# Kernel tuning notes

Hardware: AMD Instinct MI355X
Metric: run time of the kernel (lower is better)

Reference implementation:

```python
import jax, jax.numpy as jnp
import numpy as np
import math

D_MODEL = 1024
N_HEADS = 16
D_FF = 4096
D_K = D_MODEL // N_HEADS
B, S = 2, 2048
EPS = 1e-5


def _linear_params(key, fan_in, fan_out):
    kw, kb = jax.random.split(key)
    bound = 1.0 / math.sqrt(fan_in)
    W = jax.random.uniform(kw, (fan_out, fan_in), jnp.float32, -bound, bound)
    b = jax.random.uniform(kb, (fan_out,), jnp.float32, -bound, bound)
    return W, b


def setup_inputs() -> dict:
    key = jax.random.key(0)
    ks = jax.random.split(key, 8)
    x = jax.random.normal(ks[0], (B, S, D_MODEL), jnp.float32)
    # causal mask, broadcast over batch and heads; 0 -> masked
    mask = jnp.tril(jnp.ones((S, S), jnp.int32))[None, None, :, :]
    wq, bq = _linear_params(ks[1], D_MODEL, D_MODEL)
    wk, bk = _linear_params(ks[2], D_MODEL, D_MODEL)
    wv, bv = _linear_params(ks[3], D_MODEL, D_MODEL)
    wo, bo = _linear_params(ks[4], D_MODEL, D_MODEL)
    w1, b1 = _linear_params(ks[5], D_MODEL, D_FF)
    w2, b2 = _linear_params(ks[6], D_FF, D_MODEL)
    g1 = jnp.ones((D_MODEL,), jnp.float32)
    be1 = jnp.zeros((D_MODEL,), jnp.float32)
    g2 = jnp.ones((D_MODEL,), jnp.float32)
    be2 = jnp.zeros((D_MODEL,), jnp.float32)
    return dict(x=x, mask=mask, wq=wq, bq=bq, wk=wk, bk=bk, wv=wv, bv=bv,
                wo=wo, bo=bo, w1=w1, b1=b1, w2=w2, b2=b2,
                g1=g1, be1=be1, g2=g2, be2=be2)


def _layernorm(x, g, b):
    mu = jnp.mean(x, axis=-1, keepdims=True)
    var = jnp.mean(jnp.square(x - mu), axis=-1, keepdims=True)
    return (x - mu) * jax.lax.rsqrt(var + EPS) * g + b


def reference(x, mask, wq, bq, wk, bk, wv, bv, wo, bo, w1, b1, w2, b2, g1, be1, g2, be2):
    Bsz, Sl, _ = x.shape
    def heads(t):  # [B,S,D] -> [B,H,S,d_k]
        return t.reshape(Bsz, Sl, N_HEADS, D_K).transpose(0, 2, 1, 3)
    Q = heads(x @ wq.T + bq)
    K = heads(x @ wk.T + bk)
    V = heads(x @ wv.T + bv)
    scores = jnp.einsum('bhqd,bhkd->bhqk', Q, K) / math.sqrt(D_K)
    scores = jnp.where(mask == 0, jnp.float32(-1e9), scores)
    attn = jax.nn.softmax(scores, axis=-1)
    out = jnp.einsum('bhqk,bhkd->bhqd', attn, V)
    out = out.transpose(0, 2, 1, 3).reshape(Bsz, Sl, D_MODEL)
    attn_out = out @ wo.T + bo
    h = _layernorm(x + attn_out, g1, be1)  # dropout is identity in eval
    ff = jax.nn.relu(h @ w1.T + b1) @ w2.T + b2
    return _layernorm(h + ff, g2, be2)
```

## Files before the change

### kernel.cpp

```cpp
#include <hip/hip_runtime.h>
#include <hip/hip_bf16.h>


using f32x4 = __attribute__((ext_vector_type(4))) float;
using s16x8 = __attribute__((ext_vector_type(8))) short;

constexpr int D_MODEL = 1024;
constexpr int D_FF    = 4096;
constexpr int DK      = 64;
constexpr int BB      = 2;
constexpr int SS      = 2048;
constexpr int NTOK    = BB * SS;

#define QSCALE 0.18033688011112042f

__device__ __forceinline__ ushort f2bf(float f) {
    unsigned u = __float_as_uint(f);
    u += 0x7fffu + ((u >> 16) & 1u);
    return (ushort)(u >> 16);
}

__device__ __forceinline__ float ex2(float x) {
    float r;
    asm("v_exp_f32 %0, %1" : "=v"(r) : "v"(x));
    return r;
}

__device__ __forceinline__ void gload_lds16(const void* g, void* l) {
    __builtin_amdgcn_global_load_lds(
        (const __attribute__((address_space(1))) void*)g,
        (__attribute__((address_space(3))) void*)l, 16, 0, 0);
}

struct CvtArgs { const float* src[7]; ushort* dst[7]; };

__global__ __launch_bounds__(256) void cvt_all(CvtArgs a) {
    constexpr long S[8] = {0L<<20, 1L<<20, 2L<<20, 3L<<20,
                           4L<<20, 8L<<20, 12L<<20, 16L<<20};
    long i = ((long)blockIdx.x * 256 + threadIdx.x) * 4;
    int s = 0;
#pragma unroll
    for (int j = 1; j < 7; ++j) if (i >= S[j]) s = j;
    long off = i - S[s];
    float4 v = *(const float4*)(a.src[s] + off);
    ushort4 o;
    o.x = f2bf(v.x); o.y = f2bf(v.y); o.z = f2bf(v.z); o.w = f2bf(v.w);
    *(ushort4*)(a.dst[s] + off) = o;
}

template <bool RELU, bool OUTBF16, bool BIASROW, bool SCALEQ>
__global__ __launch_bounds__(256, 2) void gemm_bt(
        const ushort* __restrict__ A, const ushort* __restrict__ W,
        const float* __restrict__ bias, const float* __restrict__ bias2, int nsplit,
        void* __restrict__ Cout, int M, int N, int Klen, int ldk, int gx, int splitk) {
    __shared__ __align__(16) char Asb[2][128 * 128];
    __shared__ __align__(16) char Bsb[2][128 * 128];

    const int nwg = (int)gridDim.x;
    const int id  = (int)blockIdx.x;
    const int sw  = (id & 7) * (nwg >> 3) + (id >> 3);
    const int tps = nwg / splitk;
    const int s   = sw / tps;
    const int rem = sw - s * tps;
    const int bx  = rem % gx, by = rem / gx;

    const int t  = threadIdx.x;
    const int l  = t & 63;
    const int w  = t >> 6;
    const int wr = w >> 1, wc = w & 1;
    const int li = l & 15, g = l >> 4;
    const int bm0 = by << 7;
    const int bn0 = bx << 7;
    const int kbase = s * Klen;

    f32x4 acc[4][4];
#pragma unroll
    for (int m = 0; m < 4; ++m)
#pragma unroll
        for (int n = 0; n < 4; ++n)
            acc[m][n] = (f32x4){0.f, 0.f, 0.f, 0.f};

    const int rsub = l >> 3, slot = l & 7;
    const int swzel = (((slot * 16) ^ (rsub << 4)) >> 1);

    auto stage = [&](int buf, int k0) {
#pragma unroll
        for (int i = 0; i < 4; ++i) {
            const int rbase = i * 32 + w * 8;
            gload_lds16(A + (size_t)(bm0 + rbase + rsub) * ldk + kbase + k0 + swzel,
                        Asb[buf] + rbase * 128);
            gload_lds16(W + (size_t)(bn0 + rbase + rsub) * ldk + kbase + k0 + swzel,
                        Bsb[buf] + rbase * 128);
        }
    };

    const int nk = Klen >> 6;
    stage(0, 0);
    __syncthreads();

    for (int tt = 0; tt < nk; ++tt) {
        const int cur = tt & 1;
        if (tt + 1 < nk) stage(cur ^ 1, (tt + 1) << 6);
#pragma unroll
        for (int ks = 0; ks < 2; ++ks) {
            s16x8 af[4], bfr[4];
#pragma unroll
            for (int m = 0; m < 4; ++m) {
                int row = wr * 64 + m * 16 + li;
                af[m] = *(const s16x8*)(Asb[cur] + row * 128 + (((ks * 4 + g) * 16) ^ ((row & 7) << 4)));
            }
#pragma unroll
            for (int n = 0; n < 4; ++n) {
                int row = wc * 64 + n * 16 + li;
                bfr[n] = *(const s16x8*)(Bsb[cur] + row * 128 + (((ks * 4 + g) * 16) ^ ((row & 7) << 4)));
            }
            __builtin_amdgcn_s_setprio(1);
#pragma unroll
            for (int m = 0; m < 4; ++m)
#pragma unroll
                for (int n = 0; n < 4; ++n)
                    acc[m][n] = __builtin_amdgcn_mfma_f32_16x16x32_bf16(af[m], bfr[n], acc[m][n], 0, 0, 0);
            __builtin_amdgcn_s_setprio(0);
        }
        __syncthreads();
    }

    const float* bptr = (s == 0) ? bias : nullptr;
    float* Cf = (float*)Cout + (size_t)s * M * N;
#pragma unroll
    for (int m = 0; m < 4; ++m) {
        int row0 = bm0 + wr * 64 + m * 16 + g * 4;
#pragma unroll
        for (int n = 0; n < 4; ++n) {
            int col = bn0 + wc * 64 + n * 16 + li;
            float bsv = 0.f;
            if (!BIASROW && bptr) bsv = (col < nsplit) ? bptr[col] : bias2[col - nsplit];
#pragma unroll
            for (int r = 0; r < 4; ++r) {
                float v = acc[m][n][r] + (BIASROW ? (bptr ? bptr[row0 + r] : 0.f) : bsv);
                if (RELU) v = fmaxf(v, 0.f);
                if (SCALEQ && col < nsplit) v *= QSCALE;
                size_t idx = (size_t)(row0 + r) * N + col;
                if (OUTBF16) ((ushort*)Cout)[idx] = f2bf(v);
                else         Cf[idx] = v;
            }
        }
    }
}

__global__ __launch_bounds__(256, 4) void attn_kernel(
        const ushort* __restrict__ QKb, const ushort* __restrict__ VtG,
        ushort* __restrict__ ctx) {
    __shared__ __align__(16) char Ks[2][64 * 128];
    __shared__ __align__(16) char Vs[2][64 * 128];
    __shared__ __align__(16) char Ps[4][16 * 128];

    const int t  = threadIdx.x;
    const int l  = t & 63;
    const int w  = t >> 6;
    const int li = l & 15, g = l >> 4;
    const int bx = (int)blockIdx.x;
    const int h  = blockIdx.y;
    const int b  = blockIdx.z;

    const ushort* Kp = QKb + (size_t)(b * SS) * 2048 + 1024 + h * DK;
    const ushort* Vp = VtG + (size_t)(h * DK) * NTOK + b * SS;

    const int rsub = l >> 3, slot = l & 7;
    const int swzsrc = (slot * 16) ^ (rsub << 4);

    auto stage = [&](int buf, int kt) {
#pragma unroll
        for (int c = 0; c < 2; ++c) {
            int row0 = (w + c * 4) * 8;
            gload_lds16((const char*)(Kp + (size_t)(kt + row0 + rsub) * 2048) + swzsrc,
                        Ks[buf] + row0 * 128);
            gload_lds16((const char*)(Vp + (size_t)(row0 + rsub) * NTOK + kt) + swzsrc,
                        Vs[buf] + row0 * 128);
        }
    };

    char* Pw = Ps[w];
    const int rswz = (li & 7) << 4;

    for (int ss = 0; ss < 2; ++ss) {
        const int stripe = ss ? bx : (SS / 64 - 1 - bx);
        const int qb = stripe * 64;
        const int qw = qb + w * 16;

        const ushort* Qp = QKb + (size_t)(b * SS + qw) * 2048 + h * DK;
        s16x8 qf[2];
#pragma unroll
        for (int ds = 0; ds < 2; ++ds)
            qf[ds] = *(const s16x8*)(Qp + li * 2048 + ds * 32 + g * 8);

        f32x4 o[4];
#pragma unroll
        for (int d = 0; d < 4; ++d) o[d] = (f32x4){0.f, 0.f, 0.f, 0.f};
        float m_ = -1e30f, ls = 0.f;

        const int nt = stripe + 1;
        stage(0, 0);
        __syncthreads();

        for (int tt = 0; tt < nt; ++tt) {
            const int kt = tt * 64;
            const int cur = tt & 1;
            if (tt + 1 < nt) stage(cur ^ 1, kt + 64);

            f32x4 sa[4];
#pragma unroll
            for (int ks = 0; ks < 4; ++ks) sa[ks] = (f32x4){0.f, 0.f, 0.f, 0.f};
#pragma unroll
            for (int ks = 0; ks < 4; ++ks) {
                int row = ks * 16 + li;
#pragma unroll
                for (int ds = 0; ds < 2; ++ds) {
                    s16x8 kf = *(const s16x8*)(Ks[cur] + row * 128 + ((ds * 64 + g * 16) ^ rswz));
                    __builtin_amdgcn_s_setprio(1);
                    sa[ks] = __builtin_amdgcn_mfma_f32_16x16x32_bf16(kf, qf[ds], sa[ks], 0, 0, 0);
                    __builtin_amdgcn_s_setprio(0);
                }
            }

            const bool maskt = (tt == nt - 1);
            float p[4][4];
            float pmax = -1e30f;
#pragma unroll
            for (int ks = 0; ks < 4; ++ks)
#pragma unroll
                for (int r = 0; r < 4; ++r) {
                    float sv = sa[ks][r];
                    if (maskt && (kt + ks * 16 + g * 4 + r > qw + li)) sv = -1e30f;
                    p[ks][r] = sv;
                    pmax = fmaxf(pmax, sv);
                }

            if (!__all(pmax <= m_ + 11.5f)) {
                float mx = fmaxf(pmax, __shfl_xor(pmax, 16));
                mx = fmaxf(mx, __shfl_xor(mx, 32));
                float nm = fmaxf(m_, mx);
                float fs = ex2(m_ - nm);
                m_ = nm;
                ls *= fs;
                float fsr[4];
#pragma unroll
                for (int r = 0; r < 4; ++r) fsr[r] = __shfl(fs, g * 4 + r);
#pragma unroll
                for (int d = 0; d < 4; ++d)
#pragma unroll
                    for (int r = 0; r < 4; ++r) o[d][r] *= fsr[r];
            }
            float rs = 0.f;
#pragma unroll
            for (int ks = 0; ks < 4; ++ks)
#pragma unroll
                for (int r = 0; r < 4; ++r) {
                    p[ks][r] = ex2(p[ks][r] - m_);
                    rs += p[ks][r];
                }
            rs += __shfl_xor(rs, 16);
            rs += __shfl_xor(rs, 32);
            ls += rs;

#pragma unroll
            for (int ks = 0; ks < 4; ++ks) {
                uint u0, u1;
                asm("v_cvt_pk_bf16_f32 %0, %1, %2" : "=v"(u0) : "v"(p[ks][0]), "v"(p[ks][1]));
                asm("v_cvt_pk_bf16_f32 %0, %1, %2" : "=v"(u1) : "v"(p[ks][2]), "v"(p[ks][3]));
                uint2 uv; uv.x = u0; uv.y = u1;
                *(uint2*)(Pw + li * 128 + ((ks * 32 + g * 8) ^ ((li & 7) << 4))) = uv;
            }

            s16x8 pf[2];
#pragma unroll
            for (int ks2 = 0; ks2 < 2; ++ks2)
                pf[ks2] = *(const s16x8*)(Pw + li * 128 + ((ks2 * 64 + g * 16) ^ ((li & 7) << 4)));
#pragma unroll
            for (int dblk = 0; dblk < 4; ++dblk) {
                int vrow = dblk * 16 + li;
#pragma unroll
                for (int ks2 = 0; ks2 < 2; ++ks2) {
                    s16x8 vf = *(const s16x8*)(Vs[cur] + vrow * 128 + ((ks2 * 64 + g * 16) ^ rswz));
                    __builtin_amdgcn_s_setprio(1);
                    o[dblk] = __builtin_amdgcn_mfma_f32_16x16x32_bf16(pf[ks2], vf, o[dblk], 0, 0, 0);
                    __builtin_amdgcn_s_setprio(0);
                }
            }
            __syncthreads();
        }

        float lsr[4];
#pragma unroll
        for (int r = 0; r < 4; ++r) lsr[r] = __shfl(ls, g * 4 + r);
#pragma unroll
        for (int r = 0; r < 4; ++r) {
            float inv = 1.0f / lsr[r];
            ushort* cp = ctx + (size_t)(b * SS + qw + g * 4 + r) * D_MODEL + h * DK;
#pragma unroll
            for (int dblk = 0; dblk < 4; ++dblk)
                cp[dblk * 16 + li] = f2bf(o[dblk][r] * inv);
        }
    }
}

template <bool WBF, bool X3>
__global__ __launch_bounds__(256) void ln_fused(
        const float* __restrict__ xa, const float* __restrict__ xb,
        const float* __restrict__ xc,
        const float* __restrict__ gamma, const float* __restrict__ beta,
        float* __restrict__ outf, ushort* __restrict__ outb) {
    const int row = blockIdx.x;
    const int t   = threadIdx.x;
    const size_t off = (size_t)row * D_MODEL + t * 4;
    float4 a = *(const float4*)(xa + off);
    float4 c = *(const float4*)(xb + off);
    float z0 = a.x + c.x, z1 = a.y + c.y, z2 = a.z + c.z, z3 = a.w + c.w;
    if constexpr (X3) {
        float4 d = *(const float4*)(xc + off);
        z0 += d.x; z1 += d.y; z2 += d.z; z3 += d.w;
    }
    float sum = z0 + z1 + z2 + z3;
    float sq  = z0 * z0 + z1 * z1 + z2 * z2 + z3 * z3;
#pragma unroll
    for (int o = 1; o < 64; o <<= 1) {
        sum += __shfl_xor(sum, o);
        sq  += __shfl_xor(sq, o);
    }
    __shared__ float s1[4], s2[4];
    if ((t & 63) == 0) { s1[t >> 6] = sum; s2[t >> 6] = sq; }
    __syncthreads();
    float tot = s1[0] + s1[1] + s1[2] + s1[3];
    float tsq = s2[0] + s2[1] + s2[2] + s2[3];
    const float invn = 1.0f / (float)D_MODEL;
    float mu  = tot * invn;
    float var = tsq * invn - mu * mu;
    float rstd = rsqrtf(var + 1e-5f);
    float4 gv = *(const float4*)(gamma + t * 4);
    float4 bv = *(const float4*)(beta + t * 4);
    float y0 = (z0 - mu) * rstd * gv.x + bv.x;
    float y1 = (z1 - mu) * rstd * gv.y + bv.y;
    float y2 = (z2 - mu) * rstd * gv.z + bv.z;
    float y3 = (z3 - mu) * rstd * gv.w + bv.w;
    float4 y = {y0, y1, y2, y3};
    *(float4*)(outf + off) = y;
    if constexpr (WBF) {
        ushort4 u;
        u.x = f2bf(y0); u.y = f2bf(y1); u.z = f2bf(y2); u.w = f2bf(y3);
        *(ushort4*)(outb + off) = u;
    }
}

extern "C" void kernel_launch(void* const* d_in, const int* in_sizes, int n_in,
                              void* d_out, int out_size, void* d_ws, size_t ws_size,
                              hipStream_t stream) {
    const float* x   = (const float*)d_in[0];
    const float* wq  = (const float*)d_in[2];  const float* bq  = (const float*)d_in[3];
    const float* wk  = (const float*)d_in[4];  const float* bk  = (const float*)d_in[5];
    const float* wv  = (const float*)d_in[6];  const float* bv  = (const float*)d_in[7];
    const float* wo  = (const float*)d_in[8];  const float* bo  = (const float*)d_in[9];
    const float* w1  = (const float*)d_in[10]; const float* b1  = (const float*)d_in[11];
    const float* w2  = (const float*)d_in[12]; const float* b2  = (const float*)d_in[13];
    const float* g1  = (const float*)d_in[14]; const float* be1 = (const float*)d_in[15];
    const float* g2  = (const float*)d_in[16]; const float* be2 = (const float*)d_in[17];
    float* out = (float*)d_out;

    char* ws = (char*)d_ws;
    const size_t MB = 1u << 20;
    ushort* wqkb = (ushort*)(ws + 0 * MB);
    ushort* wvb  = (ushort*)(ws + 4 * MB);
    ushort* wob  = (ushort*)(ws + 6 * MB);
    ushort* w1b  = (ushort*)(ws + 8 * MB);
    ushort* w2b  = (ushort*)(ws + 16 * MB);
    ushort* xb   = (ushort*)(ws + 24 * MB);
    ushort* QKb  = (ushort*)(ws + 32 * MB);
    ushort* VtG  = (ushort*)(ws + 48 * MB);
    ushort* ctx  = (ushort*)(ws + 56 * MB);
    float*  p0   = (float*)(ws + 64 * MB);
    float*  p1   = (float*)(ws + 80 * MB);
    float*  h    = (float*)(ws + 96 * MB);
    ushort* hb   = (ushort*)(ws + 112 * MB);
    ushort* ffib = (ushort*)(ws + 24 * MB);

    CvtArgs ca;
    ca.src[0] = wq; ca.dst[0] = wqkb;
    ca.src[1] = wk; ca.dst[1] = wqkb + D_MODEL * D_MODEL;
    ca.src[2] = wv; ca.dst[2] = wvb;
    ca.src[3] = wo; ca.dst[3] = wob;
    ca.src[4] = w1; ca.dst[4] = w1b;
    ca.src[5] = w2; ca.dst[5] = w2b;
    ca.src[6] = x;  ca.dst[6] = xb;
    cvt_all<<<dim3(16384), dim3(256), 0, stream>>>(ca);

    dim3 blk(256);
    gemm_bt<false, true, false, true><<<dim3(512), blk, 0, stream>>>(
        xb, wqkb, bq, bk, D_MODEL, QKb, NTOK, 2 * D_MODEL, D_MODEL, D_MODEL, 16, 1);
    gemm_bt<false, true, true, false><<<dim3(256), blk, 0, stream>>>(
        wvb, xb, bv, bv, 0, VtG, D_MODEL, NTOK, D_MODEL, D_MODEL, 32, 1);

    attn_kernel<<<dim3(SS / 128, 16, BB), dim3(256), 0, stream>>>(QKb, VtG, ctx);

    gemm_bt<false, false, false, false><<<dim3(512), blk, 0, stream>>>(
        ctx, wob, bo, bo, D_MODEL, p0, NTOK, D_MODEL, 512, D_MODEL, 8, 2);
    ln_fused<true, true><<<dim3(NTOK), blk, 0, stream>>>(x, p0, p1, g1, be1, h, hb);

    gemm_bt<true, true, false, false><<<dim3(1024), blk, 0, stream>>>(
        hb, w1b, b1, b1, D_FF, ffib, NTOK, D_FF, D_MODEL, D_MODEL, 32, 1);
    gemm_bt<false, false, false, false><<<dim3(512), blk, 0, stream>>>(
        ffib, w2b, b2, b2, D_MODEL, p0, NTOK, D_MODEL, 2048, D_FF, 8, 2);
    ln_fused<false, true><<<dim3(NTOK), blk, 0, stream>>>(h, p0, p1, g2, be2, out, nullptr);
}
```

Baseline: 248.0 us.

## Widen attention KV tile to 128 keys per iteration with new V LDS layout

The attention kernel now processes 128 keys per loop iteration instead of 64. It doubles the K/V shared-memory staging buffers and changes the swizzled V layout to 256-byte rows, which halves the number of barriers, stage calls and online-softmax rescale checks per query stripe. In exchange, LDS use roughly doubles and register pressure rises (launch bounds drop from 4 to 2 blocks per CU), reducing occupancy. When the tile count is odd, the last iteration also computes up to 64 extra masked keys.

```diff
diff --git a/kernel.cpp b/kernel.cpp
--- a/kernel.cpp
+++ b/kernel.cpp
@@ -148,12 +148,12 @@
     }
 }
 
-__global__ __launch_bounds__(256, 4) void attn_kernel(
+__global__ __launch_bounds__(256, 2) void attn_kernel(
         const ushort* __restrict__ QKb, const ushort* __restrict__ VtG,
         ushort* __restrict__ ctx) {
-    __shared__ __align__(16) char Ks[2][64 * 128];
-    __shared__ __align__(16) char Vs[2][64 * 128];
-    __shared__ __align__(16) char Ps[4][16 * 128];
+    __shared__ __align__(16) char Ks[2][128 * 128];
+    __shared__ __align__(16) char Vs[2][64 * 256];
+    __shared__ __align__(16) char Ps[4][2][2048];
 
     const int t  = threadIdx.x;
     const int l  = t & 63;
@@ -167,20 +167,24 @@
     const ushort* Vp = VtG + (size_t)(h * DK) * NTOK + b * SS;
 
     const int rsub = l >> 3, slot = l & 7;
-    const int swzsrc = (slot * 16) ^ (rsub << 4);
+    const int swzK = (slot * 16) ^ (rsub << 4);
+    const int vrl  = l >> 4;
+    const int svzbase = (l & 15) * 16;
 
     auto stage = [&](int buf, int kt) {
 #pragma unroll
-        for (int c = 0; c < 2; ++c) {
-            int row0 = (w + c * 4) * 8;
-            gload_lds16((const char*)(Kp + (size_t)(kt + row0 + rsub) * 2048) + swzsrc,
-                        Ks[buf] + row0 * 128);
-            gload_lds16((const char*)(Vp + (size_t)(row0 + rsub) * NTOK + kt) + swzsrc,
-                        Vs[buf] + row0 * 128);
+        for (int c = 0; c < 4; ++c) {
+            int kr0 = (w + c * 4) * 8;
+            gload_lds16((const char*)(Kp + (size_t)(kt + kr0 + rsub) * 2048) + swzK,
+                        Ks[buf] + kr0 * 128);
+            int vr0 = (w + c * 4) * 4;
+            int vr  = vr0 + vrl;
+            int svz = (svzbase ^ ((vr & 7) << 4)) >> 1;
+            gload_lds16(Vp + (size_t)vr * NTOK + kt + svz,
+                        Vs[buf] + vr0 * 256);
         }
     };
 
-    char* Pw = Ps[w];
     const int rswz = (li & 7) << 4;
 
     for (int ss = 0; ss < 2; ++ss) {
@@ -200,41 +204,44 @@
         float m_ = -1e30f, ls = 0.f;
 
         const int nt = stripe + 1;
+        const int ni = (nt + 1) >> 1;
         stage(0, 0);
         __syncthreads();
 
-        for (int tt = 0; tt < nt; ++tt) {
-            const int kt = tt * 64;
-            const int cur = tt & 1;
-            if (tt + 1 < nt) stage(cur ^ 1, kt + 64);
-
-            f32x4 sa[4];
-#pragma unroll
-            for (int ks = 0; ks < 4; ++ks) sa[ks] = (f32x4){0.f, 0.f, 0.f, 0.f};
-#pragma unroll
-            for (int ks = 0; ks < 4; ++ks) {
-                int row = ks * 16 + li;
+        for (int it = 0; it < ni; ++it) {
+            const int kt = it * 128;
+            const int cur = it & 1;
+            if (it + 1 < ni) stage(cur ^ 1, kt + 128);
+
+            f32x4 sa[8];
+#pragma unroll
+            for (int kk = 0; kk < 8; ++kk) sa[kk] = (f32x4){0.f, 0.f, 0.f, 0.f};
+#pragma unroll
+            for (int kk = 0; kk < 8; ++kk) {
+                int row = kk * 16 + li;
 #pragma unroll
                 for (int ds = 0; ds < 2; ++ds) {
                     s16x8 kf = *(const s16x8*)(Ks[cur] + row * 128 + ((ds * 64 + g * 16) ^ rswz));
                     __builtin_amdgcn_s_setprio(1);
-                    sa[ks] = __builtin_amdgcn_mfma_f32_16x16x32_bf16(kf, qf[ds], sa[ks], 0, 0, 0);
+                    sa[kk] = __builtin_amdgcn_mfma_f32_16x16x32_bf16(kf, qf[ds], sa[kk], 0, 0, 0);
                     __builtin_amdgcn_s_setprio(0);
                 }
             }
 
-            const bool maskt = (tt == nt - 1);
-            float p[4][4];
+            const bool maskt = (it == ni - 1);
+            float p[8][4];
             float pmax = -1e30f;
 #pragma unroll
-            for (int ks = 0; ks < 4; ++ks)
+            for (int kk = 0; kk < 8; ++kk) {
 #pragma unroll
                 for (int r = 0; r < 4; ++r) {
-                    float sv = sa[ks][r];
-                    if (maskt && (kt + ks * 16 + g * 4 + r > qw + li)) sv = -1e30f;
-                    p[ks][r] = sv;
-                    pmax = fmaxf(pmax, sv);
+                    float sv = sa[kk][r];
+                    if (maskt && (kt + kk * 16 + g * 4 + r > qw + li)) sv = -1e30f;
+                    p[kk][r] = sv;
                 }
+                float a = fmaxf(fmaxf(p[kk][0], p[kk][1]), fmaxf(p[kk][2], p[kk][3]));
+                pmax = fmaxf(pmax, a);
+            }
 
             if (!__all(pmax <= m_ + 11.5f)) {
                 float mx = fmaxf(pmax, __shfl_xor(pmax, 16));
@@ -253,38 +260,46 @@
             }
             float rs = 0.f;
 #pragma unroll
-            for (int ks = 0; ks < 4; ++ks)
+            for (int kk = 0; kk < 8; ++kk) {
+                float s0 = 0.f;
 #pragma unroll
                 for (int r = 0; r < 4; ++r) {
-                    p[ks][r] = ex2(p[ks][r] - m_);
-                    rs += p[ks][r];
+                    p[kk][r] = ex2(p[kk][r] - m_);
+                    s0 += p[kk][r];
                 }
+                rs += s0;
+            }
             rs += __shfl_xor(rs, 16);
             rs += __shfl_xor(rs, 32);
             ls += rs;
 
 #pragma unroll
-            for (int ks = 0; ks < 4; ++ks) {
-                uint u0, u1;
-                asm("v_cvt_pk_bf16_f32 %0, %1, %2" : "=v"(u0) : "v"(p[ks][0]), "v"(p[ks][1]));
-                asm("v_cvt_pk_bf16_f32 %0, %1, %2" : "=v"(u1) : "v"(p[ks][2]), "v"(p[ks][3]));
-                uint2 uv; uv.x = u0; uv.y = u1;
-                *(uint2*)(Pw + li * 128 + ((ks * 32 + g * 8) ^ ((li & 7) << 4))) = uv;
-            }
-
-            s16x8 pf[2];
-#pragma unroll
-            for (int ks2 = 0; ks2 < 2; ++ks2)
-                pf[ks2] = *(const s16x8*)(Pw + li * 128 + ((ks2 * 64 + g * 16) ^ ((li & 7) << 4)));
-#pragma unroll
-            for (int dblk = 0; dblk < 4; ++dblk) {
-                int vrow = dblk * 16 + li;
-#pragma unroll
-                for (int ks2 = 0; ks2 < 2; ++ks2) {
-                    s16x8 vf = *(const s16x8*)(Vs[cur] + vrow * 128 + ((ks2 * 64 + g * 16) ^ rswz));
-                    __builtin_amdgcn_s_setprio(1);
-                    o[dblk] = __builtin_amdgcn_mfma_f32_16x16x32_bf16(pf[ks2], vf, o[dblk], 0, 0, 0);
-                    __builtin_amdgcn_s_setprio(0);
+            for (int hf = 0; hf < 2; ++hf) {
+                char* Pw = Ps[w][hf];
+#pragma unroll
+                for (int ks = 0; ks < 4; ++ks) {
+                    int kk = hf * 4 + ks;
+                    uint u0, u1;
+                    asm("v_cvt_pk_bf16_f32 %0, %1, %2" : "=v"(u0) : "v"(p[kk][0]), "v"(p[kk][1]));
+                    asm("v_cvt_pk_bf16_f32 %0, %1, %2" : "=v"(u1) : "v"(p[kk][2]), "v"(p[kk][3]));
+                    uint2 uv; uv.x = u0; uv.y = u1;
+                    *(uint2*)(Pw + li * 128 + ((ks * 32 + g * 8) ^ rswz)) = uv;
+                }
+                s16x8 pf[2];
+#pragma unroll
+                for (int ks2 = 0; ks2 < 2; ++ks2)
+                    pf[ks2] = *(const s16x8*)(Pw + li * 128 + ((ks2 * 64 + g * 16) ^ rswz));
+#pragma unroll
+                for (int dblk = 0; dblk < 4; ++dblk) {
+                    int vrow = dblk * 16 + li;
+#pragma unroll
+                    for (int ks2 = 0; ks2 < 2; ++ks2) {
+                        s16x8 vf = *(const s16x8*)(Vs[cur] + vrow * 256 +
+                                       ((hf * 128 + ks2 * 64 + g * 16) ^ ((vrow & 7) << 4)));
+                        __builtin_amdgcn_s_setprio(1);
+                        o[dblk] = __builtin_amdgcn_mfma_f32_16x16x32_bf16(pf[ks2], vf, o[dblk], 0, 0, 0);
+                        __builtin_amdgcn_s_setprio(0);
+                    }
                 }
             }
             __syncthreads();
```

Measured after the change: 248.4 us. No clear change (+0.2%).

## Split attention KV range into two halves with combine pass; merge QK and V^T GEMMs

Applied to the files above, without the earlier changes.

The attention kernel now splits each query stripe's key range into two halves across a doubled grid z-dimension. Each half writes unnormalized bf16 partial outputs plus running max and sum, and a new combine kernel merges them into ctx. This is meant to raise parallelism and balance work across CUs for the causal attention. The QK and V-transpose projections are also fused into one 768-block launch to cut a launch and fill the GPU better. The cost is an extra kernel, an extra round-trip through global memory for partials, and bf16 rounding of the unnormalized partials.

```diff
diff --git a/kernel.cpp b/kernel.cpp
--- a/kernel.cpp
+++ b/kernel.cpp
@@ -20,6 +20,9 @@
     return (ushort)(u >> 16);
 }
 
+__device__ __forceinline__ float bflo(uint v) { return __uint_as_float(v << 16); }
+__device__ __forceinline__ float bfhi(uint v) { return __uint_as_float(v & 0xffff0000u); }
+
 __device__ __forceinline__ float ex2(float x) {
     float r;
     asm("v_exp_f32 %0, %1" : "=v"(r) : "v"(x));
@@ -48,10 +51,10 @@
     *(ushort4*)(a.dst[s] + off) = o;
 }
 
-template <bool RELU, bool OUTBF16, bool BIASROW, bool SCALEQ>
+template <bool RELU, bool OUTBF16>
 __global__ __launch_bounds__(256, 2) void gemm_bt(
         const ushort* __restrict__ A, const ushort* __restrict__ W,
-        const float* __restrict__ bias, const float* __restrict__ bias2, int nsplit,
+        const float* __restrict__ bias,
         void* __restrict__ Cout, int M, int N, int Klen, int ldk, int gx, int splitk) {
     __shared__ __align__(16) char Asb[2][128 * 128];
     __shared__ __align__(16) char Bsb[2][128 * 128];
@@ -125,7 +128,7 @@
         __syncthreads();
     }
 
-    const float* bptr = (s == 0) ? bias : nullptr;
+    const bool dobias = (s == 0);
     float* Cf = (float*)Cout + (size_t)s * M * N;
 #pragma unroll
     for (int m = 0; m < 4; ++m) {
@@ -133,13 +136,11 @@
 #pragma unroll
         for (int n = 0; n < 4; ++n) {
             int col = bn0 + wc * 64 + n * 16 + li;
-            float bsv = 0.f;
-            if (!BIASROW && bptr) bsv = (col < nsplit) ? bptr[col] : bias2[col - nsplit];
+            float bsv = dobias ? bias[col] : 0.f;
 #pragma unroll
             for (int r = 0; r < 4; ++r) {
-                float v = acc[m][n][r] + (BIASROW ? (bptr ? bptr[row0 + r] : 0.f) : bsv);
+                float v = acc[m][n][r] + bsv;
                 if (RELU) v = fmaxf(v, 0.f);
-                if (SCALEQ && col < nsplit) v *= QSCALE;
                 size_t idx = (size_t)(row0 + r) * N + col;
                 if (OUTBF16) ((ushort*)Cout)[idx] = f2bf(v);
                 else         Cf[idx] = v;
@@ -148,9 +149,110 @@
     }
 }
 
+__global__ __launch_bounds__(256, 2) void gemm_qkvt(
+        const ushort* __restrict__ xb, const ushort* __restrict__ wqkb,
+        const ushort* __restrict__ wvb,
+        const float* __restrict__ bq, const float* __restrict__ bk,
+        const float* __restrict__ bv,
+        ushort* __restrict__ QKb, ushort* __restrict__ VtG) {
+    __shared__ __align__(16) char Asb[2][128 * 128];
+    __shared__ __align__(16) char Bsb[2][128 * 128];
+
+    const int id = (int)blockIdx.x;
+    const int sw = (id & 7) * 96 + (id >> 3);
+    const bool vt = (sw >= 512);
+    int bx, by, N;
+    const ushort *A, *W;
+    if (!vt) { bx = sw % 16;          by = sw / 16;          A = xb;  W = wqkb; N = 2048; }
+    else     { int s2 = sw - 512; bx = s2 % 32; by = s2 / 32; A = wvb; W = xb;  N = 4096; }
+
+    const int t  = threadIdx.x;
+    const int l  = t & 63;
+    const int w  = t >> 6;
+    const int wr = w >> 1, wc = w & 1;
+    const int li = l & 15, g = l >> 4;
+    const int bm0 = by << 7;
+    const int bn0 = bx << 7;
+
+    f32x4 acc[4][4];
+#pragma unroll
+    for (int m = 0; m < 4; ++m)
+#pragma unroll
+        for (int n = 0; n < 4; ++n)
+            acc[m][n] = (f32x4){0.f, 0.f, 0.f, 0.f};
+
+    const int rsub = l >> 3, slot = l & 7;
+    const int swzel = (((slot * 16) ^ (rsub << 4)) >> 1);
+
+    auto stage = [&](int buf, int k0) {
+#pragma unroll
+        for (int i = 0; i < 4; ++i) {
+            const int rbase = i * 32 + w * 8;
+            gload_lds16(A + (size_t)(bm0 + rbase + rsub) * 1024 + k0 + swzel,
+                        Asb[buf] + rbase * 128);
+            gload_lds16(W + (size_t)(bn0 + rbase + rsub) * 1024 + k0 + swzel,
+                        Bsb[buf] + rbase * 128);
+        }
+    };
+
+    stage(0, 0);
+    __syncthreads();
+
+    for (int tt = 0; tt < 16; ++tt) {
+        const int cur = tt & 1;
+        if (tt + 1 < 16) stage(cur ^ 1, (tt + 1) << 6);
+#pragma unroll
+        for (int ks = 0; ks < 2; ++ks) {
+            s16x8 af[4], bfr[4];
+#pragma unroll
+            for (int m = 0; m < 4; ++m) {
+                int row = wr * 64 + m * 16 + li;
+                af[m] = *(const s16x8*)(Asb[cur] + row * 128 + (((ks * 4 + g) * 16) ^ ((row & 7) << 4)));
+            }
+#pragma unroll
+            for (int n = 0; n < 4; ++n) {
+                int row = wc * 64 + n * 16 + li;
+                bfr[n] = *(const s16x8*)(Bsb[cur] + row * 128 + (((ks * 4 + g) * 16) ^ ((row & 7) << 4)));
+            }
+            __builtin_amdgcn_s_setprio(1);
+#pragma unroll
+            for (int m = 0; m < 4; ++m)
+#pragma unroll
+                for (int n = 0; n < 4; ++n)
+                    acc[m][n] = __builtin_amdgcn_mfma_f32_16x16x32_bf16(af[m], bfr[n], acc[m][n], 0, 0, 0);
+            __builtin_amdgcn_s_setprio(0);
+        }
+        __syncthreads();
+    }
+
+#pragma unroll
+    for (int m = 0; m < 4; ++m) {
+        int row0 = bm0 + wr * 64 + m * 16 + g * 4;
+#pragma unroll
+        for (int n = 0; n < 4; ++n) {
+            int col = bn0 + wc * 64 + n * 16 + li;
+            if (!vt) {
+                float bsv = (col < 1024) ? bq[col] : bk[col - 1024];
+                float sc  = (col < 1024) ? QSCALE : 1.f;
+#pragma unroll
+                for (int r = 0; r < 4; ++r) {
+                    float v = (acc[m][n][r] + bsv) * sc;
+                    QKb[(size_t)(row0 + r) * 2048 + col] = f2bf(v);
+                }
+            } else {
+#pragma unroll
+                for (int r = 0; r < 4; ++r) {
+                    float v = acc[m][n][r] + bv[row0 + r];
+                    VtG[(size_t)(row0 + r) * 4096 + col] = f2bf(v);
+                }
+            }
+        }
+    }
+}
+
 __global__ __launch_bounds__(256, 4) void attn_kernel(
         const ushort* __restrict__ QKb, const ushort* __restrict__ VtG,
-        ushort* __restrict__ ctx) {
+        ushort* __restrict__ po, float* __restrict__ ml) {
     __shared__ __align__(16) char Ks[2][64 * 128];
     __shared__ __align__(16) char Vs[2][64 * 128];
     __shared__ __align__(16) char Ps[4][16 * 128];
@@ -161,7 +263,9 @@
     const int li = l & 15, g = l >> 4;
     const int bx = (int)blockIdx.x;
     const int h  = blockIdx.y;
-    const int b  = blockIdx.z;
+    const int z  = (int)blockIdx.z;
+    const int b    = z & 1;
+    const int half = z >> 1;
 
     const ushort* Kp = QKb + (size_t)(b * SS) * 2048 + 1024 + h * DK;
     const ushort* Vp = VtG + (size_t)(h * DK) * NTOK + b * SS;
@@ -199,109 +303,141 @@
         for (int d = 0; d < 4; ++d) o[d] = (f32x4){0.f, 0.f, 0.f, 0.f};
         float m_ = -1e30f, ls = 0.f;
 
-        const int nt = stripe + 1;
-        stage(0, 0);
-        __syncthreads();
-
-        for (int tt = 0; tt < nt; ++tt) {
-            const int kt = tt * 64;
-            const int cur = tt & 1;
-            if (tt + 1 < nt) stage(cur ^ 1, kt + 64);
-
-            f32x4 sa[4];
-#pragma unroll
-            for (int ks = 0; ks < 4; ++ks) sa[ks] = (f32x4){0.f, 0.f, 0.f, 0.f};
-#pragma unroll
-            for (int ks = 0; ks < 4; ++ks) {
-                int row = ks * 16 + li;
-#pragma unroll
-                for (int ds = 0; ds < 2; ++ds) {
-                    s16x8 kf = *(const s16x8*)(Ks[cur] + row * 128 + ((ds * 64 + g * 16) ^ rswz));
-                    __builtin_amdgcn_s_setprio(1);
-                    sa[ks] = __builtin_amdgcn_mfma_f32_16x16x32_bf16(kf, qf[ds], sa[ks], 0, 0, 0);
-                    __builtin_amdgcn_s_setprio(0);
+        const int ntt  = stripe + 1;
+        const int tbeg = half ? (ntt >> 1) : 0;
+        const int tend = half ? ntt : (ntt >> 1);
+        const int ntH  = tend - tbeg;
+
+        if (ntH > 0) {
+            stage(0, tbeg * 64);
+            __syncthreads();
+
+            for (int tt = 0; tt < ntH; ++tt) {
+                const int kt = (tbeg + tt) * 64;
+                const int cur = tt & 1;
+                if (tt + 1 < ntH) stage(cur ^ 1, kt + 64);
+
+                f32x4 sa[4];
+#pragma unroll
+                for (int ks = 0; ks < 4; ++ks) sa[ks] = (f32x4){0.f, 0.f, 0.f, 0.f};
+#pragma unroll
+                for (int ks = 0; ks < 4; ++ks) {
+                    int row = ks * 16 + li;
+#pragma unroll
+                    for (int ds = 0; ds < 2; ++ds) {
+                        s16x8 kf = *(const s16x8*)(Ks[cur] + row * 128 + ((ds * 64 + g * 16) ^ rswz));
+                        __builtin_amdgcn_s_setprio(1);
+                        sa[ks] = __builtin_amdgcn_mfma_f32_16x16x32_bf16(kf, qf[ds], sa[ks], 0, 0, 0);
+                        __builtin_amdgcn_s_setprio(0);
+                    }
                 }
-            }
-
-            const bool maskt = (tt == nt - 1);
-            float p[4][4];
-            float pmax = -1e30f;
-#pragma unroll
-            for (int ks = 0; ks < 4; ++ks)
-#pragma unroll
-                for (int r = 0; r < 4; ++r) {
-                    float sv = sa[ks][r];
-                    if (maskt && (kt + ks * 16 + g * 4 + r > qw + li)) sv = -1e30f;
-                    p[ks][r] = sv;
-                    pmax = fmaxf(pmax, sv);
+
+                const bool maskt = (tbeg + tt == ntt - 1);
+                float p[4][4];
+                float pmax = -1e30f;
+#pragma unroll
+                for (int ks = 0; ks < 4; ++ks)
+#pragma unroll
+                    for (int r = 0; r < 4; ++r) {
+                        float sv = sa[ks][r];
+                        if (maskt && (kt + ks * 16 + g * 4 + r > qw + li)) sv = -1e30f;
+                        p[ks][r] = sv;
+                        pmax = fmaxf(pmax, sv);
+                    }
+
+                if (!__all(pmax <= m_ + 11.5f)) {
+                    float mx = fmaxf(pmax, __shfl_xor(pmax, 16));
+                    mx = fmaxf(mx, __shfl_xor(mx, 32));
+                    float nm = fmaxf(m_, mx);
+                    float fs = ex2(m_ - nm);
+                    m_ = nm;
+                    ls *= fs;
+                    float fsr[4];
+#pragma unroll
+                    for (int r = 0; r < 4; ++r) fsr[r] = __shfl(fs, g * 4 + r);
+#pragma unroll
+                    for (int d = 0; d < 4; ++d)
+#pragma unroll
+                        for (int r = 0; r < 4; ++r) o[d][r] *= fsr[r];
                 }
-
-            if (!__all(pmax <= m_ + 11.5f)) {
-                float mx = fmaxf(pmax, __shfl_xor(pmax, 16));
-                mx = fmaxf(mx, __shfl_xor(mx, 32));
-                float nm = fmaxf(m_, mx);
-                float fs = ex2(m_ - nm);
-                m_ = nm;
-                ls *= fs;
-                float fsr[4];
-#pragma unroll
-                for (int r = 0; r < 4; ++r) fsr[r] = __shfl(fs, g * 4 + r);
-#pragma unroll
-                for (int d = 0; d < 4; ++d)
-#pragma unroll
-                    for (int r = 0; r < 4; ++r) o[d][r] *= fsr[r];
-            }
-            float rs = 0.f;
-#pragma unroll
-            for (int ks = 0; ks < 4; ++ks)
-#pragma unroll
-                for (int r = 0; r < 4; ++r) {
-                    p[ks][r] = ex2(p[ks][r] - m_);
-                    rs += p[ks][r];
+                float rs = 0.f;
+#pragma unroll
+                for (int ks = 0; ks < 4; ++ks)
+#pragma unroll
+                    for (int r = 0; r < 4; ++r) {
+                        p[ks][r] = ex2(p[ks][r] - m_);
+                        rs += p[ks][r];
+                    }
+                rs += __shfl_xor(rs, 16);
+                rs += __shfl_xor(rs, 32);
+                ls += rs;
+
+#pragma unroll
+                for (int ks = 0; ks < 4; ++ks) {
+                    uint u0, u1;
+                    asm("v_cvt_pk_bf16_f32 %0, %1, %2" : "=v"(u0) : "v"(p[ks][0]), "v"(p[ks][1]));
+                    asm("v_cvt_pk_bf16_f32 %0, %1, %2" : "=v"(u1) : "v"(p[ks][2]), "v"(p[ks][3]));
+                    uint2 uv; uv.x = u0; uv.y = u1;
+                    *(uint2*)(Pw + li * 128 + ((ks * 32 + g * 8) ^ rswz)) = uv;
                 }
-            rs += __shfl_xor(rs, 16);
-            rs += __shfl_xor(rs, 32);
-            ls += rs;
-
-#pragma unroll
-            for (int ks = 0; ks < 4; ++ks) {
-                uint u0, u1;
-                asm("v_cvt_pk_bf16_f32 %0, %1, %2" : "=v"(u0) : "v"(p[ks][0]), "v"(p[ks][1]));
-                asm("v_cvt_pk_bf16_f32 %0, %1, %2" : "=v"(u1) : "v"(p[ks][2]), "v"(p[ks][3]));
-                uint2 uv; uv.x = u0; uv.y = u1;
-                *(uint2*)(Pw + li * 128 + ((ks * 32 + g * 8) ^ ((li & 7) << 4))) = uv;
-            }
-
-            s16x8 pf[2];
-#pragma unroll
-            for (int ks2 = 0; ks2 < 2; ++ks2)
-                pf[ks2] = *(const s16x8*)(Pw + li * 128 + ((ks2 * 64 + g * 16) ^ ((li & 7) << 4)));
-#pragma unroll
-            for (int dblk = 0; dblk < 4; ++dblk) {
-                int vrow = dblk * 16 + li;
-#pragma unroll
-                for (int ks2 = 0; ks2 < 2; ++ks2) {
-                    s16x8 vf = *(const s16x8*)(Vs[cur] + vrow * 128 + ((ks2 * 64 + g * 16) ^ rswz));
-                    __builtin_amdgcn_s_setprio(1);
-                    o[dblk] = __builtin_amdgcn_mfma_f32_16x16x32_bf16(pf[ks2], vf, o[dblk], 0, 0, 0);
-                    __builtin_amdgcn_s_setprio(0);
+
+                s16x8 pf[2];
+#pragma unroll
+                for (int ks2 = 0; ks2 < 2; ++ks2)
+                    pf[ks2] = *(const s16x8*)(Pw + li * 128 + ((ks2 * 64 + g * 16) ^ rswz));
+#pragma unroll
+                for (int dblk = 0; dblk < 4; ++dblk) {
+                    int vrow = dblk * 16 + li;
+#pragma unroll
+                    for (int ks2 = 0; ks2 < 2; ++ks2) {
+                        s16x8 vf = *(const s16x8*)(Vs[cur] + vrow * 128 + ((ks2 * 64 + g * 16) ^ rswz));
+                        __builtin_amdgcn_s_setprio(1);
+                        o[dblk] = __builtin_amdgcn_mfma_f32_16x16x32_bf16(pf[ks2], vf, o[dblk], 0, 0, 0);
+                        __builtin_amdgcn_s_setprio(0);
+                    }
                 }
-            }
-            __syncthreads();
-        }
-
-        float lsr[4];
-#pragma unroll
-        for (int r = 0; r < 4; ++r) lsr[r] = __shfl(ls, g * 4 + r);
+                __syncthreads();
+            }
+        }
+
 #pragma unroll
         for (int r = 0; r < 4; ++r) {
-            float inv = 1.0f / lsr[r];
-            ushort* cp = ctx + (size_t)(b * SS + qw + g * 4 + r) * D_MODEL + h * DK;
+            ushort* pp = po + ((((size_t)(half * 2 + b)) * SS + qw + g * 4 + r) * 16 + h) * 64;
 #pragma unroll
             for (int dblk = 0; dblk < 4; ++dblk)
-                cp[dblk * 16 + li] = f2bf(o[dblk][r] * inv);
-        }
-    }
+                pp[dblk * 16 + li] = f2bf(o[dblk][r]);
+        }
+        if (l < 16) {
+            size_t mrow = (((size_t)(half * 2 + b)) * SS + qw + l) * 16 + h;
+            ml[mrow * 2]     = m_;
+            ml[mrow * 2 + 1] = ls;
+        }
+    }
+}
+
+__global__ __launch_bounds__(256) void attn_combine(
+        const ushort* __restrict__ po, const float* __restrict__ ml,
+        ushort* __restrict__ ctx) {
+    const int idx = blockIdx.x * 256 + threadIdx.x;
+    const int row = idx >> 4;
+    const int d4  = (idx & 15) * 4;
+    const int HR  = 2 * SS * 16;
+
+    float m0 = ml[(size_t)row * 2],        l0 = ml[(size_t)row * 2 + 1];
+    float m1 = ml[(size_t)(HR + row) * 2], l1 = ml[(size_t)(HR + row) * 2 + 1];
+    float mx = fmaxf(m0, m1);
+    float w0 = ex2(m0 - mx), w1 = ex2(m1 - mx);
+    float inv = 1.0f / (l0 * w0 + l1 * w1);
+
+    uint2 a = *(const uint2*)(po + (size_t)row * 64 + d4);
+    uint2 c = *(const uint2*)(po + (size_t)(HR + row) * 64 + d4);
+    float v0 = (bflo(a.x) * w0 + bflo(c.x) * w1) * inv;
+    float v1 = (bfhi(a.x) * w0 + bfhi(c.x) * w1) * inv;
+    float v2 = (bflo(a.y) * w0 + bflo(c.y) * w1) * inv;
+    float v3 = (bfhi(a.y) * w0 + bfhi(c.y) * w1) * inv;
+    ushort4 o;
+    o.x = f2bf(v0); o.y = f2bf(v1); o.z = f2bf(v2); o.w = f2bf(v3);
+    *(ushort4*)(ctx + (size_t)(row >> 4) * 1024 + (row & 15) * 64 + d4) = o;
 }
 
 template <bool WBF, bool X3>
@@ -376,6 +512,8 @@
     ushort* QKb  = (ushort*)(ws + 32 * MB);
     ushort* VtG  = (ushort*)(ws + 48 * MB);
     ushort* ctx  = (ushort*)(ws + 56 * MB);
+    ushort* po   = (ushort*)(ws + 64 * MB);
+    float*  ml   = (float*)(ws + 81 * MB);
     float*  p0   = (float*)(ws + 64 * MB);
     float*  p1   = (float*)(ws + 80 * MB);
     float*  h    = (float*)(ws + 96 * MB);
@@ -393,20 +531,18 @@
     cvt_all<<<dim3(16384), dim3(256), 0, stream>>>(ca);
 
     dim3 blk(256);
-    gemm_bt<false, true, false, true><<<dim3(512), blk, 0, stream>>>(
-        xb, wqkb, bq, bk, D_MODEL, QKb, NTOK, 2 * D_MODEL, D_MODEL, D_MODEL, 16, 1);
-    gemm_bt<false, true, true, false><<<dim3(256), blk, 0, stream>>>(
-        wvb, xb, bv, bv, 0, VtG, D_MODEL, NTOK, D_MODEL, D_MODEL, 32, 1);
-
-    attn_kernel<<<dim3(SS / 128, 16, BB), dim3(256), 0, stream>>>(QKb, VtG, ctx);
-
-    gemm_bt<false, false, false, false><<<dim3(512), blk, 0, stream>>>(
-        ctx, wob, bo, bo, D_MODEL, p0, NTOK, D_MODEL, 512, D_MODEL, 8, 2);
+    gemm_qkvt<<<dim3(768), blk, 0, stream>>>(xb, wqkb, wvb, bq, bk, bv, QKb, VtG);
+
+    attn_kernel<<<dim3(SS / 128, 16, 2 * BB), blk, 0, stream>>>(QKb, VtG, po, ml);
+    attn_combine<<<dim3(4096), blk, 0, stream>>>(po, ml, ctx);
+
+    gemm_bt<false, false><<<dim3(512), blk, 0, stream>>>(
+        ctx, wob, bo, p0, NTOK, D_MODEL, 512, D_MODEL, 8, 2);
     ln_fused<true, true><<<dim3(NTOK), blk, 0, stream>>>(x, p0, p1, g1, be1, h, hb);
 
-    gemm_bt<true, true, false, false><<<dim3(1024), blk, 0, stream>>>(
-        hb, w1b, b1, b1, D_FF, ffib, NTOK, D_FF, D_MODEL, D_MODEL, 32, 1);
-    gemm_bt<false, false, false, false><<<dim3(512), blk, 0, stream>>>(
-        ffib, w2b, b2, b2, D_MODEL, p0, NTOK, D_MODEL, 2048, D_FF, 8, 2);
+    gemm_bt<true, true><<<dim3(1024), blk, 0, stream>>>(
+        hb, w1b, b1, ffib, NTOK, D_FF, D_MODEL, D_MODEL, 32, 1);
+    gemm_bt<false, false><<<dim3(512), blk, 0, stream>>>(
+        ffib, w2b, b2, p0, NTOK, D_MODEL, 2048, D_FF, 8, 2);
     ln_fused<false, true><<<dim3(NTOK), blk, 0, stream>>>(h, p0, p1, g2, be2, out, nullptr);
 }
```

After: 245.5 us. About the same (-1.0%).
